# Performance work log

Measured on AMD Instinct MI355X. Metric: run time of the kernel, lower is better.

Reference implementation:

```python
import jax, jax.numpy as jnp
import numpy as np

NUM_EMBEDDINGS = 1024
EMBEDDING_DIM = 256


def setup_inputs() -> dict:
    key = jax.random.key(0)
    k1, k2 = jax.random.split(key)
    z = jax.random.normal(k1, (32, EMBEDDING_DIM, 32, 32), dtype=jnp.float32)
    codebook = jax.random.normal(k2, (NUM_EMBEDDINGS, EMBEDDING_DIM), dtype=jnp.float32)
    return {"z": z, "codebook": codebook}


def reference(z, codebook):
    # z: (B, C, H, W) -> (B, H, W, C) -> (B*H*W, C)
    B, C, H, W = z.shape
    z_bhwc = jnp.transpose(z, (0, 2, 3, 1))
    z_flat = z_bhwc.reshape(-1, C)  # (N, C)

    # pairwise squared distances: ||z||^2 + ||e||^2 - 2 z.e^T  -> (N, K)
    distances = (
        jnp.sum(z_flat ** 2, axis=1, keepdims=True)
        + jnp.sum(codebook ** 2, axis=1)
        - 2.0 * jnp.matmul(z_flat, codebook.T)
    )
    argmin_codewords = jnp.argmin(distances, axis=1)  # (N,)
    min_codewords = jax.nn.one_hot(argmin_codewords, NUM_EMBEDDINGS, dtype=jnp.float32)  # (N, K)

    # quantized latents via one-hot @ codebook, back to (B, C, H, W)
    z_quantized = jnp.matmul(min_codewords, codebook).reshape(B, H, W, C)
    z_quantized = jnp.transpose(z_quantized, (0, 3, 1, 2))
    return (min_codewords, z_quantized)
```

## Files before the change

### kernel.cpp

```cpp
#include <hip/hip_runtime.h>

#define N_ROWS 32768
#define K_CODES 1024
#define CDIM 256

typedef _Float16 half8 __attribute__((ext_vector_type(8)));
typedef _Float16 half4 __attribute__((ext_vector_type(4)));
typedef float floatx16 __attribute__((ext_vector_type(16)));
typedef unsigned long long ull;

#define WS_ZH   0ull
#define WS_ZL   16777216ull
#define WS_CBH  33554432ull
#define WS_CBL  34078720ull
#define WS_CBN  34603008ull
#define WS_PART 34607104ull
#define WS_IDX  36704256ull
#define WS_NEED 36835328ull

__device__ __forceinline__ void g2lds16(const void* g, void* l) {
    __builtin_amdgcn_global_load_lds(
        (const __attribute__((address_space(1))) void*)g,
        (__attribute__((address_space(3))) void*)l, 16, 0, 0);
}

__global__ __launch_bounds__(256) void prep_all(const float* __restrict__ z,
                                                const float* __restrict__ cb,
                                                _Float16* __restrict__ zh,
                                                _Float16* __restrict__ zl,
                                                _Float16* __restrict__ cbh,
                                                _Float16* __restrict__ cbl,
                                                float* __restrict__ cbn,
                                                ull* __restrict__ part) {
    __shared__ float t[64][68];
    if (blockIdx.x >= 2048) {
        int k = ((blockIdx.x - 2048) << 2) | (threadIdx.x >> 6);
        int lane = threadIdx.x & 63;
        float4 v = reinterpret_cast<const float4*>(cb + k * CDIM)[lane];
        float s0 = v.x * 32.f, s1 = v.y * 32.f, s2 = v.z * 32.f, s3 = v.w * 32.f;
        half4 hv, lv;
        hv[0] = (_Float16)s0; lv[0] = (_Float16)(s0 - (float)hv[0]);
        hv[1] = (_Float16)s1; lv[1] = (_Float16)(s1 - (float)hv[1]);
        hv[2] = (_Float16)s2; lv[2] = (_Float16)(s2 - (float)hv[2]);
        hv[3] = (_Float16)s3; lv[3] = (_Float16)(s3 - (float)hv[3]);
        size_t off = (size_t)((lane >> 1) * K_CODES + k) * 8 + ((lane & 1) * 4);
        *reinterpret_cast<half4*>(&cbh[off]) = hv;
        *reinterpret_cast<half4*>(&cbl[off]) = lv;
        float s = s0 * s0 + s1 * s1 + s2 * s2 + s3 * s3;
        #pragma unroll
        for (int off2 = 32; off2 > 0; off2 >>= 1) s += __shfl_down(s, off2);
        if (lane == 0) cbn[k] = s;
        return;
    }
    if (threadIdx.x < 16) part[blockIdx.x * 16 + threadIdx.x] = ~0ull;

    int hwt = blockIdx.x & 15;
    int ct  = (blockIdx.x >> 4) & 3;
    int bb  = blockIdx.x >> 6;
    int tid = threadIdx.x;
    #pragma unroll
    for (int p = 0; p < 4; p++) {
        int e = p * 256 + tid;
        int c = e >> 4, h4 = e & 15;
        float4 v = *reinterpret_cast<const float4*>(
            &z[((bb * 256 + ct * 64 + c) << 10) + hwt * 64 + h4 * 4]);
        *reinterpret_cast<float4*>(&t[c][h4 * 4]) = v;
    }
    __syncthreads();
    #pragma unroll
    for (int p = 0; p < 4; p++) {
        int e = p * 256 + tid;
        int hw = e >> 4, c4 = e & 15;
        half4 hv, lv;
        #pragma unroll
        for (int j = 0; j < 4; j++) {
            float s = t[c4 * 4 + j][hw] * 32.f;
            _Float16 h = (_Float16)s;
            hv[j] = h;
            lv[j] = (_Float16)(s - (float)h);
        }
        int n = bb * 1024 + hwt * 64 + hw;
        int cg = ct * 64 + c4 * 4;
        size_t off = (size_t)((cg >> 3) * N_ROWS + n) * 8 + (cg & 7);
        *reinterpret_cast<half4*>(&zh[off]) = hv;
        *reinterpret_cast<half4*>(&zl[off]) = lv;
    }
}

__global__ __launch_bounds__(256, 2) void vq_breg(
    const _Float16* __restrict__ zh, const _Float16* __restrict__ zl,
    const _Float16* __restrict__ cbh, const _Float16* __restrict__ cbl,
    const float* __restrict__ cbn, ull* __restrict__ part) {

    __shared__ _Float16 BhL[16384], BlL[16384];

    const int tid = threadIdx.x;
    const int lane = tid & 63, w = tid >> 6;
    const int fm = lane & 31, fq = lane >> 5;
    const int L = (blockIdx.x & 7) * 256 + (blockIdx.x >> 3);
    const int codeTile = L & 15;
    const int rowTile  = L >> 4;
    const int rowBase = rowTile * 256, codeBase = codeTile * 64;

    #pragma unroll
    for (int p = 0; p < 8; p++) {
        int G = p * 256 + tid;
        int plane = G >> 6, code = G & 63;
        size_t so = ((size_t)plane * K_CODES + codeBase + code) * 8;
        g2lds16(cbh + so, &BhL[G * 8]);
        g2lds16(cbl + so, &BlL[G * 8]);
    }

    float cbnv[2];
    #pragma unroll
    for (int j = 0; j < 2; j++) cbnv[j] = cbn[codeBase + j * 32 + fm];

    floatx16 acc[4];
    #pragma unroll
    for (int i = 0; i < 4; i++) acc[i] = (floatx16)0.f;

    __syncthreads();

    const int rw = rowBase + w * 64;
    #pragma unroll
    for (int cc = 0; cc < 8; cc++) {
        #pragma unroll
        for (int s = 0; s < 2; s++) {
            const int plane = cc * 4 + s * 2 + fq;
            half8 ah[2], al[2], bh[2], bl[2];
            #pragma unroll
            for (int i = 0; i < 2; i++) {
                size_t ao = ((size_t)plane * N_ROWS + rw + i * 32 + fm) * 8;
                ah[i] = *reinterpret_cast<const half8*>(&zh[ao]);
                al[i] = *reinterpret_cast<const half8*>(&zl[ao]);
            }
            #pragma unroll
            for (int j = 0; j < 2; j++) {
                int gb = (plane * 64 + j * 32 + fm) * 8;
                bh[j] = *reinterpret_cast<const half8*>(&BhL[gb]);
                bl[j] = *reinterpret_cast<const half8*>(&BlL[gb]);
            }
            #pragma unroll
            for (int i = 0; i < 2; i++)
                #pragma unroll
                for (int j = 0; j < 2; j++) {
                    acc[i*2+j] = __builtin_amdgcn_mfma_f32_32x32x16_f16(ah[i], bh[j], acc[i*2+j], 0, 0, 0);
                    acc[i*2+j] = __builtin_amdgcn_mfma_f32_32x32x16_f16(al[i], bh[j], acc[i*2+j], 0, 0, 0);
                    acc[i*2+j] = __builtin_amdgcn_mfma_f32_32x32x16_f16(ah[i], bl[j], acc[i*2+j], 0, 0, 0);
                }
        }
    }

    #pragma unroll
    for (int i = 0; i < 2; i++)
        #pragma unroll
        for (int r = 0; r < 16; r++) {
            float best = 3.4e38f; int bcode = 0x7fffffff;
            #pragma unroll
            for (int j = 0; j < 2; j++) {
                float d = fmaf(-2.f, acc[i*2+j][r], cbnv[j]);
                int code = codeBase + j * 32 + fm;
                if (d < best) { best = d; bcode = code; }
            }
            #pragma unroll
            for (int m = 1; m < 32; m <<= 1) {
                float ov = __shfl_xor(best, m, 64);
                int   oc = __shfl_xor(bcode, m, 64);
                if (ov < best || (ov == best && oc < bcode)) { best = ov; bcode = oc; }
            }
            if (fm == 0) {
                int row = rw + i * 32 + (r & 3) + 8 * (r >> 2) + 4 * fq;
                unsigned u = __float_as_uint(best);
                u = (u & 0x80000000u) ? ~u : (u | 0x80000000u);
                atomicMin(&part[row], ((ull)u << 32) | (unsigned)bcode);
            }
        }
}

__global__ __launch_bounds__(256) void onehot_fin3(const ull* __restrict__ part,
                                                   int* __restrict__ idx,
                                                   float* __restrict__ out) {
    __shared__ int sid[16];
    const int rb = blockIdx.x * 16;
    const int tid = threadIdx.x;
    if (tid < 16) {
        int id = (int)(part[rb + tid] & 0xffffffffu);
        sid[tid] = id;
        idx[rb + tid] = id;
    }
    __syncthreads();
    const int k4 = tid << 2;
    #pragma unroll
    for (int r = 0; r < 16; r++) {
        int id = sid[r];
        float4 v4;
        v4.x = (k4     == id) ? 1.f : 0.f;
        v4.y = (k4 + 1 == id) ? 1.f : 0.f;
        v4.z = (k4 + 2 == id) ? 1.f : 0.f;
        v4.w = (k4 + 3 == id) ? 1.f : 0.f;
        reinterpret_cast<float4*>(out)[(size_t)(rb + r) * 256 + tid] = v4;
    }
}

__global__ __launch_bounds__(256) void zq_fill2(const int* __restrict__ idx,
                                                const float* __restrict__ cb,
                                                float* __restrict__ out) {
    __shared__ float tile[64][257];
    const int tid = threadIdx.x;
    const int n0 = (blockIdx.x >> 2) << 8;
    const int c0 = (blockIdx.x & 3) << 6;
    const int b  = n0 >> 10;
    const int hw0 = n0 & 1023;

    const int id = idx[n0 + tid];
    const float4* cb4 = reinterpret_cast<const float4*>(cb);
    #pragma unroll
    for (int jj = 0; jj < 16; jj++) {
        float4 v = cb4[id * 64 + (c0 >> 2) + jj];
        tile[jj * 4 + 0][tid] = v.x;
        tile[jj * 4 + 1][tid] = v.y;
        tile[jj * 4 + 2][tid] = v.z;
        tile[jj * 4 + 3][tid] = v.w;
    }
    __syncthreads();
    #pragma unroll
    for (int c = 0; c < 64; c++) {
        out[((size_t)(b * 256 + c0 + c) << 10) + hw0 + tid] = tile[c][tid];
    }
}


__global__ __launch_bounds__(64) void cb_norms(const float* __restrict__ cb,
                                               float* __restrict__ cbn) {
    int k = blockIdx.x;
    int lane = threadIdx.x;
    float4 v = reinterpret_cast<const float4*>(cb + k * CDIM)[lane];
    float s = v.x * v.x + v.y * v.y + v.z * v.z + v.w * v.w;
    #pragma unroll
    for (int off = 32; off > 0; off >>= 1) s += __shfl_down(s, off);
    if (lane == 0) cbn[k] = s;
}

__global__ __launch_bounds__(256) void cb_transpose(const float* __restrict__ cb,
                                                    float* __restrict__ cbt) {
    __shared__ float t[32][33];
    int k0 = (blockIdx.x & 31) * 32;
    int c0 = (blockIdx.x >> 5) * 32;
    int lane = threadIdx.x & 31;
    int row = threadIdx.x >> 5;
    #pragma unroll
    for (int s = 0; s < 4; s++) {
        int r = row + s * 8;
        t[r][lane] = cb[(k0 + r) * CDIM + c0 + lane];
    }
    __syncthreads();
    #pragma unroll
    for (int s = 0; s < 4; s++) {
        int r = row + s * 8;
        cbt[(c0 + r) * K_CODES + k0 + lane] = t[lane][r];
    }
}

__global__ __launch_bounds__(512, 2) void vq_argmin(const float* __restrict__ z,
                                                    const float* __restrict__ cbt,
                                                    const float* __restrict__ cbn,
                                                    int* __restrict__ idx_out) {
    __shared__ float As[64][128];
    __shared__ float Bs[64][256];

    const int tid = threadIdx.x;
    const int tx = tid & 31;
    const int ty = tid >> 5;
    const int rowBase = blockIdx.x * 128;
    const int bb = rowBase >> 10;
    const int hwBase = rowBase & 1023;

    float minv[8];
    int   mini[8];
    #pragma unroll
    for (int i = 0; i < 8; i++) { minv[i] = 3.4e38f; mini[i] = 0; }

    for (int kt = 0; kt < K_CODES; kt += 256) {
        float acc[2][2][4][4];
        #pragma unroll
        for (int a = 0; a < 2; a++)
            #pragma unroll
            for (int b = 0; b < 2; b++)
                #pragma unroll
                for (int i = 0; i < 4; i++)
                    #pragma unroll
                    for (int j = 0; j < 4; j++) acc[a][b][i][j] = 0.f;

        for (int ccb = 0; ccb < CDIM; ccb += 64) {
            #pragma unroll
            for (int l = 0; l < 4; l++) {
                int f = tid + l * 512;
                int r4 = f & 31, c = f >> 5;
                float4 v = *reinterpret_cast<const float4*>(
                    &z[((bb * 256 + ccb + c) << 10) + hwBase + r4 * 4]);
                *reinterpret_cast<float4*>(&As[c][r4 * 4]) = v;
            }
            #pragma unroll
            for (int l = 0; l < 8; l++) {
                int f = tid + l * 512;
                int k4 = f & 63, c = f >> 6;
                float4 v = *reinterpret_cast<const float4*>(
                    &cbt[(ccb + c) * K_CODES + kt + k4 * 4]);
                *reinterpret_cast<float4*>(&Bs[c][k4 * 4]) = v;
            }
            __syncthreads();
            #pragma unroll 4
            for (int c = 0; c < 64; c++) {
                float4 a0 = *reinterpret_cast<const float4*>(&As[c][ty * 4]);
                float4 a1 = *reinterpret_cast<const float4*>(&As[c][64 + ty * 4]);
                float4 b0 = *reinterpret_cast<const float4*>(&Bs[c][tx * 4]);
                float4 b1 = *reinterpret_cast<const float4*>(&Bs[c][128 + tx * 4]);
                float av[2][4] = {{a0.x, a0.y, a0.z, a0.w}, {a1.x, a1.y, a1.z, a1.w}};
                float bw[2][4] = {{b0.x, b0.y, b0.z, b0.w}, {b1.x, b1.y, b1.z, b1.w}};
                #pragma unroll
                for (int ri = 0; ri < 2; ri++)
                    #pragma unroll
                    for (int i = 0; i < 4; i++)
                        #pragma unroll
                        for (int ci = 0; ci < 2; ci++)
                            #pragma unroll
                            for (int j = 0; j < 4; j++)
                                acc[ri][ci][i][j] =
                                    fmaf(av[ri][i], bw[ci][j], acc[ri][ci][i][j]);
            }
            __syncthreads();
        }
        #pragma unroll
        for (int ci = 0; ci < 2; ci++)
            #pragma unroll
            for (int j = 0; j < 4; j++) {
                int code = kt + ci * 128 + tx * 4 + j;
                float nrm = cbn[code];
                #pragma unroll
                for (int ri = 0; ri < 2; ri++)
                    #pragma unroll
                    for (int i = 0; i < 4; i++) {
                        float d = fmaf(-2.f, acc[ri][ci][i][j], nrm);
                        int r = ri * 4 + i;
                        if (d < minv[r]) { minv[r] = d; mini[r] = code; }
                    }
            }
    }

    __syncthreads();
    float (*rv)[32] = reinterpret_cast<float(*)[32]>(&As[0][0]);
    int   (*rix)[32] = reinterpret_cast<int(*)[32]>(&As[32][0]);
    #pragma unroll
    for (int ri = 0; ri < 2; ri++)
        #pragma unroll
        for (int i = 0; i < 4; i++) {
            int row = ri * 64 + ty * 4 + i;
            rv[row][tx] = minv[ri * 4 + i];
            rix[row][tx] = mini[ri * 4 + i];
        }
    __syncthreads();
    if (tid < 128) {
        float bvv = rv[tid][0]; int bii = rix[tid][0];
        #pragma unroll
        for (int t = 1; t < 32; t++) {
            float v = rv[tid][t]; int ii = rix[tid][t];
            if (v < bvv || (v == bvv && ii < bii)) { bvv = v; bii = ii; }
        }
        idx_out[rowBase + tid] = bii;
    }
}

__global__ __launch_bounds__(256) void onehot_fill(const int* __restrict__ idx,
                                                   float* __restrict__ out) {
    int i = blockIdx.x * 256 + threadIdx.x;
    int n  = i >> 8;
    int k4 = (i & 255) << 2;
    int id = idx[n];
    float4 v;
    v.x = (k4     == id) ? 1.f : 0.f;
    v.y = (k4 + 1 == id) ? 1.f : 0.f;
    v.z = (k4 + 2 == id) ? 1.f : 0.f;
    v.w = (k4 + 3 == id) ? 1.f : 0.f;
    reinterpret_cast<float4*>(out)[i] = v;
}

extern "C" void kernel_launch(void* const* d_in, const int* in_sizes, int n_in,
                              void* d_out, int out_size, void* d_ws, size_t ws_size,
                              hipStream_t stream) {
    const float* z  = (const float*)d_in[0];
    const float* cb = (const float*)d_in[1];
    float* out0 = (float*)d_out;
    float* out1 = out0 + (size_t)N_ROWS * K_CODES;

    if (ws_size >= WS_NEED) {
        _Float16* zh  = (_Float16*)((char*)d_ws + WS_ZH);
        _Float16* zl  = (_Float16*)((char*)d_ws + WS_ZL);
        _Float16* cbh = (_Float16*)((char*)d_ws + WS_CBH);
        _Float16* cbl = (_Float16*)((char*)d_ws + WS_CBL);
        float* cbn = (float*)((char*)d_ws + WS_CBN);
        ull* part = (ull*)((char*)d_ws + WS_PART);
        int* idx = (int*)((char*)d_ws + WS_IDX);

        prep_all<<<2304, 256, 0, stream>>>(z, cb, zh, zl, cbh, cbl, cbn, part);
        vq_breg<<<2048, 256, 0, stream>>>(zh, zl, cbh, cbl, cbn, part);
        onehot_fin3<<<2048, 256, 0, stream>>>(part, idx, out0);
        zq_fill2<<<512, 256, 0, stream>>>(idx, cb, out1);
    } else {
        float* cbn = (float*)d_ws;
        int*   idx = (int*)((char*)d_ws + 4096);
        float* cbt = (float*)((char*)d_ws + 4096 + 131072);

        cb_norms<<<K_CODES, 64, 0, stream>>>(cb, cbn);
        cb_transpose<<<256, 256, 0, stream>>>(cb, cbt);
        vq_argmin<<<N_ROWS / 128, 512, 0, stream>>>(z, cbt, cbn, idx);
        onehot_fill<<<(N_ROWS * K_CODES / 4) / 256, 256, 0, stream>>>(idx, out0);
        zq_fill2<<<512, 256, 0, stream>>>(idx, cb, out1);
    }
}
```

Before: 320.5 us.

## Double-buffer A and B tiles in LDS with 128x128 block tiling

The distance GEMM kernel changes from a 256-row by 64-code tile, where the whole codebook slice sits in LDS and z is read straight from global memory, to a 128x128 tile. A 2x2 wave layout reads both z and codebook chunks from a double-buffered LDS area filled by async global-to-LDS loads. The next chunk's loads are meant to overlap the MFMA work on the current one. The smaller LDS footprint allows 4 blocks per CU instead of 2. The cost is two barriers per chunk and lower register budget under the tighter launch bounds.

```diff
diff --git a/kernel.cpp b/kernel.cpp
--- a/kernel.cpp
+++ b/kernel.cpp
@@ -87,69 +87,74 @@
     }
 }
 
-__global__ __launch_bounds__(256, 2) void vq_breg(
+__global__ __launch_bounds__(256, 4) void vq_db(
     const _Float16* __restrict__ zh, const _Float16* __restrict__ zl,
     const _Float16* __restrict__ cbh, const _Float16* __restrict__ cbl,
     const float* __restrict__ cbn, ull* __restrict__ part) {
 
-    __shared__ _Float16 BhL[16384], BlL[16384];
+    __shared__ _Float16 AhL[2][2048], AlL[2][2048];
+    __shared__ _Float16 BhL[2][2048], BlL[2][2048];
 
     const int tid = threadIdx.x;
-    const int lane = tid & 63, w = tid >> 6;
+    const int lane = tid & 63, wave = tid >> 6;
+    const int wm = wave & 1, wn = wave >> 1;
     const int fm = lane & 31, fq = lane >> 5;
     const int L = (blockIdx.x & 7) * 256 + (blockIdx.x >> 3);
-    const int codeTile = L & 15;
-    const int rowTile  = L >> 4;
-    const int rowBase = rowTile * 256, codeBase = codeTile * 64;
-
-    #pragma unroll
-    for (int p = 0; p < 8; p++) {
-        int G = p * 256 + tid;
-        int plane = G >> 6, code = G & 63;
-        size_t so = ((size_t)plane * K_CODES + codeBase + code) * 8;
-        g2lds16(cbh + so, &BhL[G * 8]);
-        g2lds16(cbl + so, &BlL[G * 8]);
+    const int codeTile = L & 7;
+    const int rowTile  = L >> 3;
+    const int rowBase = rowTile * 128, codeBase = codeTile * 128;
+
+    floatx16 acc[4];
+    #pragma unroll
+    for (int i = 0; i < 4; i++) acc[i] = (floatx16)0.f;
+
+    const int p_ = tid >> 7, r_ = tid & 127;
+    auto stage = [&](int buf, int ch) {
+        const size_t ao = ((size_t)(ch * 2 + p_) * N_ROWS + rowBase + r_) * 8;
+        const size_t bo = ((size_t)(ch * 2 + p_) * K_CODES + codeBase + r_) * 8;
+        g2lds16(zh + ao,  &AhL[buf][tid * 8]);
+        g2lds16(zl + ao,  &AlL[buf][tid * 8]);
+        g2lds16(cbh + bo, &BhL[buf][tid * 8]);
+        g2lds16(cbl + bo, &BlL[buf][tid * 8]);
+    };
+    auto compute = [&](int buf) {
+        half8 ah[2], al[2], bh[2], bl[2];
+        #pragma unroll
+        for (int i = 0; i < 2; i++) {
+            int ga = fq * 128 + wm * 64 + i * 32 + fm;
+            ah[i] = *reinterpret_cast<const half8*>(&AhL[buf][ga * 8]);
+            al[i] = *reinterpret_cast<const half8*>(&AlL[buf][ga * 8]);
+        }
+        #pragma unroll
+        for (int j = 0; j < 2; j++) {
+            int gb = fq * 128 + wn * 64 + j * 32 + fm;
+            bh[j] = *reinterpret_cast<const half8*>(&BhL[buf][gb * 8]);
+            bl[j] = *reinterpret_cast<const half8*>(&BlL[buf][gb * 8]);
+        }
+        #pragma unroll
+        for (int i = 0; i < 2; i++)
+            #pragma unroll
+            for (int j = 0; j < 2; j++) {
+                acc[i*2+j] = __builtin_amdgcn_mfma_f32_32x32x16_f16(ah[i], bh[j], acc[i*2+j], 0, 0, 0);
+                acc[i*2+j] = __builtin_amdgcn_mfma_f32_32x32x16_f16(al[i], bh[j], acc[i*2+j], 0, 0, 0);
+                acc[i*2+j] = __builtin_amdgcn_mfma_f32_32x32x16_f16(ah[i], bl[j], acc[i*2+j], 0, 0, 0);
+            }
+    };
+
+    stage(0, 0);
+    __syncthreads();
+    for (int c = 0; c < 16; c += 2) {
+        stage(1, c + 1);
+        compute(0);
+        __syncthreads();
+        if (c + 2 < 16) stage(0, c + 2);
+        compute(1);
+        __syncthreads();
     }
 
     float cbnv[2];
     #pragma unroll
-    for (int j = 0; j < 2; j++) cbnv[j] = cbn[codeBase + j * 32 + fm];
-
-    floatx16 acc[4];
-    #pragma unroll
-    for (int i = 0; i < 4; i++) acc[i] = (floatx16)0.f;
-
-    __syncthreads();
-
-    const int rw = rowBase + w * 64;
-    #pragma unroll
-    for (int cc = 0; cc < 8; cc++) {
-        #pragma unroll
-        for (int s = 0; s < 2; s++) {
-            const int plane = cc * 4 + s * 2 + fq;
-            half8 ah[2], al[2], bh[2], bl[2];
-            #pragma unroll
-            for (int i = 0; i < 2; i++) {
-                size_t ao = ((size_t)plane * N_ROWS + rw + i * 32 + fm) * 8;
-                ah[i] = *reinterpret_cast<const half8*>(&zh[ao]);
-                al[i] = *reinterpret_cast<const half8*>(&zl[ao]);
-            }
-            #pragma unroll
-            for (int j = 0; j < 2; j++) {
-                int gb = (plane * 64 + j * 32 + fm) * 8;
-                bh[j] = *reinterpret_cast<const half8*>(&BhL[gb]);
-                bl[j] = *reinterpret_cast<const half8*>(&BlL[gb]);
-            }
-            #pragma unroll
-            for (int i = 0; i < 2; i++)
-                #pragma unroll
-                for (int j = 0; j < 2; j++) {
-                    acc[i*2+j] = __builtin_amdgcn_mfma_f32_32x32x16_f16(ah[i], bh[j], acc[i*2+j], 0, 0, 0);
-                    acc[i*2+j] = __builtin_amdgcn_mfma_f32_32x32x16_f16(al[i], bh[j], acc[i*2+j], 0, 0, 0);
-                    acc[i*2+j] = __builtin_amdgcn_mfma_f32_32x32x16_f16(ah[i], bl[j], acc[i*2+j], 0, 0, 0);
-                }
-        }
-    }
+    for (int j = 0; j < 2; j++) cbnv[j] = cbn[codeBase + wn * 64 + j * 32 + fm];
 
     #pragma unroll
     for (int i = 0; i < 2; i++)
@@ -159,7 +164,7 @@
             #pragma unroll
             for (int j = 0; j < 2; j++) {
                 float d = fmaf(-2.f, acc[i*2+j][r], cbnv[j]);
-                int code = codeBase + j * 32 + fm;
+                int code = codeBase + wn * 64 + j * 32 + fm;
                 if (d < best) { best = d; bcode = code; }
             }
             #pragma unroll
@@ -169,7 +174,7 @@
                 if (ov < best || (ov == best && oc < bcode)) { best = ov; bcode = oc; }
             }
             if (fm == 0) {
-                int row = rw + i * 32 + (r & 3) + 8 * (r >> 2) + 4 * fq;
+                int row = rowBase + wm * 64 + i * 32 + (r & 3) + 8 * (r >> 2) + 4 * fq;
                 unsigned u = __float_as_uint(best);
                 u = (u & 0x80000000u) ? ~u : (u | 0x80000000u);
                 atomicMin(&part[row], ((ull)u << 32) | (unsigned)bcode);
@@ -402,7 +407,7 @@
         int* idx = (int*)((char*)d_ws + WS_IDX);
 
         prep_all<<<2304, 256, 0, stream>>>(z, cb, zh, zl, cbh, cbl, cbn, part);
-        vq_breg<<<2048, 256, 0, stream>>>(zh, zl, cbh, cbl, cbn, part);
+        vq_db<<<2048, 256, 0, stream>>>(zh, zl, cbh, cbl, cbn, part);
         onehot_fin3<<<2048, 256, 0, stream>>>(part, idx, out0);
         zq_fill2<<<512, 256, 0, stream>>>(idx, cb, out1);
     } else {
```

Measured after the change: 288.8 us. 9.9% less time.

## Halve codebook LDS staging, prefetch A fragments, fuse one-hot and gather kernels

Applied to the files above, without the earlier changes.

The distance kernel now stages the codebook tile into LDS in two halves (half the shared memory), so three blocks per CU can be resident instead of two. It also double-buffers the z hi/lo fragment loads one step ahead of the MFMA work to hide global latency. The one-hot writer and quantized-latent gather are merged into a single launch that reads indices straight from the packed argmin buffer, which removes one kernel launch and the intermediate idx array. The trade-offs are an extra pair of barriers mid-loop and more registers held for the prefetch buffers under the tighter occupancy bound.

```diff
diff --git a/kernel.cpp b/kernel.cpp
--- a/kernel.cpp
+++ b/kernel.cpp
@@ -87,12 +87,12 @@
     }
 }
 
-__global__ __launch_bounds__(256, 2) void vq_breg(
+__global__ __launch_bounds__(256, 3) void vq_areg(
     const _Float16* __restrict__ zh, const _Float16* __restrict__ zl,
     const _Float16* __restrict__ cbh, const _Float16* __restrict__ cbl,
     const float* __restrict__ cbn, ull* __restrict__ part) {
 
-    __shared__ _Float16 BhL[16384], BlL[16384];
+    __shared__ _Float16 BhL[8192], BlL[8192];
 
     const int tid = threadIdx.x;
     const int lane = tid & 63, w = tid >> 6;
@@ -101,15 +101,26 @@
     const int codeTile = L & 15;
     const int rowTile  = L >> 4;
     const int rowBase = rowTile * 256, codeBase = codeTile * 64;
-
-    #pragma unroll
-    for (int p = 0; p < 8; p++) {
-        int G = p * 256 + tid;
-        int plane = G >> 6, code = G & 63;
-        size_t so = ((size_t)plane * K_CODES + codeBase + code) * 8;
-        g2lds16(cbh + so, &BhL[G * 8]);
-        g2lds16(cbl + so, &BlL[G * 8]);
-    }
+    const int rw = rowBase + w * 64;
+
+    auto stageB = [&](int h) {
+        #pragma unroll
+        for (int p = 0; p < 4; p++) {
+            int G = p * 256 + tid;
+            int plane = G >> 6, code = G & 63;
+            size_t so = ((size_t)(h * 16 + plane) * K_CODES + codeBase + code) * 8;
+            g2lds16(cbh + so, &BhL[G * 8]);
+            g2lds16(cbl + so, &BlL[G * 8]);
+        }
+    };
+    auto loadA = [&](int s, half8 (&h)[2], half8 (&l)[2]) {
+        #pragma unroll
+        for (int i = 0; i < 2; i++) {
+            size_t ao = ((size_t)(2 * s + fq) * N_ROWS + rw + i * 32 + fm) * 8;
+            h[i] = *reinterpret_cast<const half8*>(&zh[ao]);
+            l[i] = *reinterpret_cast<const half8*>(&zl[ao]);
+        }
+    };
 
     float cbnv[2];
     #pragma unroll
@@ -119,36 +130,36 @@
     #pragma unroll
     for (int i = 0; i < 4; i++) acc[i] = (floatx16)0.f;
 
-    __syncthreads();
-
-    const int rw = rowBase + w * 64;
-    #pragma unroll
-    for (int cc = 0; cc < 8; cc++) {
-        #pragma unroll
-        for (int s = 0; s < 2; s++) {
-            const int plane = cc * 4 + s * 2 + fq;
-            half8 ah[2], al[2], bh[2], bl[2];
-            #pragma unroll
-            for (int i = 0; i < 2; i++) {
-                size_t ao = ((size_t)plane * N_ROWS + rw + i * 32 + fm) * 8;
-                ah[i] = *reinterpret_cast<const half8*>(&zh[ao]);
-                al[i] = *reinterpret_cast<const half8*>(&zl[ao]);
-            }
+    half8 pah[2][2], pal[2][2];
+    loadA(0, pah[0], pal[0]);
+    stageB(0);
+    __syncthreads();
+
+    #pragma unroll
+    for (int s = 0; s < 16; s++) {
+        const int cur = s & 1, nxt = cur ^ 1;
+        if (s == 8) {
+            __syncthreads();
+            stageB(1);
+            __syncthreads();
+        }
+        if (s < 15) loadA(s + 1, pah[nxt], pal[nxt]);
+        const int lp = (s & 7) * 2 + fq;
+        half8 bh[2], bl[2];
+        #pragma unroll
+        for (int j = 0; j < 2; j++) {
+            int gb = (lp * 64 + j * 32 + fm) * 8;
+            bh[j] = *reinterpret_cast<const half8*>(&BhL[gb]);
+            bl[j] = *reinterpret_cast<const half8*>(&BlL[gb]);
+        }
+        #pragma unroll
+        for (int i = 0; i < 2; i++)
             #pragma unroll
             for (int j = 0; j < 2; j++) {
-                int gb = (plane * 64 + j * 32 + fm) * 8;
-                bh[j] = *reinterpret_cast<const half8*>(&BhL[gb]);
-                bl[j] = *reinterpret_cast<const half8*>(&BlL[gb]);
-            }
-            #pragma unroll
-            for (int i = 0; i < 2; i++)
-                #pragma unroll
-                for (int j = 0; j < 2; j++) {
-                    acc[i*2+j] = __builtin_amdgcn_mfma_f32_32x32x16_f16(ah[i], bh[j], acc[i*2+j], 0, 0, 0);
-                    acc[i*2+j] = __builtin_amdgcn_mfma_f32_32x32x16_f16(al[i], bh[j], acc[i*2+j], 0, 0, 0);
-                    acc[i*2+j] = __builtin_amdgcn_mfma_f32_32x32x16_f16(ah[i], bl[j], acc[i*2+j], 0, 0, 0);
-                }
-        }
+                acc[i*2+j] = __builtin_amdgcn_mfma_f32_32x32x16_f16(pah[cur][i], bh[j], acc[i*2+j], 0, 0, 0);
+                acc[i*2+j] = __builtin_amdgcn_mfma_f32_32x32x16_f16(pal[cur][i], bh[j], acc[i*2+j], 0, 0, 0);
+                acc[i*2+j] = __builtin_amdgcn_mfma_f32_32x32x16_f16(pah[cur][i], bl[j], acc[i*2+j], 0, 0, 0);
+            }
     }
 
     #pragma unroll
@@ -177,42 +188,37 @@
         }
 }
 
-__global__ __launch_bounds__(256) void onehot_fin3(const ull* __restrict__ part,
-                                                   int* __restrict__ idx,
-                                                   float* __restrict__ out) {
-    __shared__ int sid[16];
-    const int rb = blockIdx.x * 16;
+__global__ __launch_bounds__(256) void finalize(const ull* __restrict__ part,
+                                                const float* __restrict__ cb,
+                                                float* __restrict__ out0,
+                                                float* __restrict__ out1) {
     const int tid = threadIdx.x;
-    if (tid < 16) {
-        int id = (int)(part[rb + tid] & 0xffffffffu);
-        sid[tid] = id;
-        idx[rb + tid] = id;
-    }
-    __syncthreads();
-    const int k4 = tid << 2;
-    #pragma unroll
-    for (int r = 0; r < 16; r++) {
-        int id = sid[r];
-        float4 v4;
-        v4.x = (k4     == id) ? 1.f : 0.f;
-        v4.y = (k4 + 1 == id) ? 1.f : 0.f;
-        v4.z = (k4 + 2 == id) ? 1.f : 0.f;
-        v4.w = (k4 + 3 == id) ? 1.f : 0.f;
-        reinterpret_cast<float4*>(out)[(size_t)(rb + r) * 256 + tid] = v4;
-    }
-}
-
-__global__ __launch_bounds__(256) void zq_fill2(const int* __restrict__ idx,
-                                                const float* __restrict__ cb,
-                                                float* __restrict__ out) {
+    if (blockIdx.x < 2048) {
+        __shared__ int sid[16];
+        const int rb = blockIdx.x * 16;
+        if (tid < 16) sid[tid] = (int)(part[rb + tid] & 0xffffffffu);
+        __syncthreads();
+        const int k4 = tid << 2;
+        #pragma unroll
+        for (int r = 0; r < 16; r++) {
+            int id = sid[r];
+            float4 v4;
+            v4.x = (k4     == id) ? 1.f : 0.f;
+            v4.y = (k4 + 1 == id) ? 1.f : 0.f;
+            v4.z = (k4 + 2 == id) ? 1.f : 0.f;
+            v4.w = (k4 + 3 == id) ? 1.f : 0.f;
+            reinterpret_cast<float4*>(out0)[(size_t)(rb + r) * 256 + tid] = v4;
+        }
+        return;
+    }
     __shared__ float tile[64][257];
-    const int tid = threadIdx.x;
-    const int n0 = (blockIdx.x >> 2) << 8;
-    const int c0 = (blockIdx.x & 3) << 6;
+    const int blk = blockIdx.x - 2048;
+    const int n0 = (blk >> 2) << 8;
+    const int c0 = (blk & 3) << 6;
     const int b  = n0 >> 10;
     const int hw0 = n0 & 1023;
 
-    const int id = idx[n0 + tid];
+    const int id = (int)(part[n0 + tid] & 0xffffffffu);
     const float4* cb4 = reinterpret_cast<const float4*>(cb);
     #pragma unroll
     for (int jj = 0; jj < 16; jj++) {
@@ -225,7 +231,7 @@
     __syncthreads();
     #pragma unroll
     for (int c = 0; c < 64; c++) {
-        out[((size_t)(b * 256 + c0 + c) << 10) + hw0 + tid] = tile[c][tid];
+        out1[((size_t)(b * 256 + c0 + c) << 10) + hw0 + tid] = tile[c][tid];
     }
 }
 
@@ -384,6 +390,33 @@
     reinterpret_cast<float4*>(out)[i] = v;
 }
 
+__global__ __launch_bounds__(256) void zq_fill2(const int* __restrict__ idx,
+                                                const float* __restrict__ cb,
+                                                float* __restrict__ out) {
+    __shared__ float tile[64][257];
+    const int tid = threadIdx.x;
+    const int n0 = (blockIdx.x >> 2) << 8;
+    const int c0 = (blockIdx.x & 3) << 6;
+    const int b  = n0 >> 10;
+    const int hw0 = n0 & 1023;
+
+    const int id = idx[n0 + tid];
+    const float4* cb4 = reinterpret_cast<const float4*>(cb);
+    #pragma unroll
+    for (int jj = 0; jj < 16; jj++) {
+        float4 v = cb4[id * 64 + (c0 >> 2) + jj];
+        tile[jj * 4 + 0][tid] = v.x;
+        tile[jj * 4 + 1][tid] = v.y;
+        tile[jj * 4 + 2][tid] = v.z;
+        tile[jj * 4 + 3][tid] = v.w;
+    }
+    __syncthreads();
+    #pragma unroll
+    for (int c = 0; c < 64; c++) {
+        out[((size_t)(b * 256 + c0 + c) << 10) + hw0 + tid] = tile[c][tid];
+    }
+}
+
 extern "C" void kernel_launch(void* const* d_in, const int* in_sizes, int n_in,
                               void* d_out, int out_size, void* d_ws, size_t ws_size,
                               hipStream_t stream) {
@@ -399,12 +432,10 @@
         _Float16* cbl = (_Float16*)((char*)d_ws + WS_CBL);
         float* cbn = (float*)((char*)d_ws + WS_CBN);
         ull* part = (ull*)((char*)d_ws + WS_PART);
-        int* idx = (int*)((char*)d_ws + WS_IDX);
 
         prep_all<<<2304, 256, 0, stream>>>(z, cb, zh, zl, cbh, cbl, cbn, part);
-        vq_breg<<<2048, 256, 0, stream>>>(zh, zl, cbh, cbl, cbn, part);
-        onehot_fin3<<<2048, 256, 0, stream>>>(part, idx, out0);
-        zq_fill2<<<512, 256, 0, stream>>>(idx, cb, out1);
+        vq_areg<<<2048, 256, 0, stream>>>(zh, zl, cbh, cbl, cbn, part);
+        finalize<<<2560, 256, 0, stream>>>(part, cb, out0, out1);
     } else {
         float* cbn = (float*)d_ws;
         int*   idx = (int*)((char*)d_ws + 4096);
```

New measurement: 280.4 us (median of 2 runs). 1.14x faster.
